# Optimization experiments

Measured on AMD Instinct MI355X. Metric: run time of the kernel, lower is better.

Reference implementation:

```python
import jax, jax.numpy as jnp
import numpy as np

N = 262144      # number of 3D points
D = 128         # in_channels
NCLS = 20       # classes
M = 10          # num_prototype
EPS = 0.05      # sinkhorn epsilon
ITERS = 3       # sinkhorn iterations
GAMMA = 0.99    # EMA momentum
LN_EPS = 1e-5

def layer_norm(x, g, b):
    mu = jnp.mean(x, axis=-1, keepdims=True)
    v = jnp.mean((x - mu) ** 2, axis=-1, keepdims=True)
    return (x - mu) / jnp.sqrt(v + LN_EPS) * g + b

def l2n(x):
    # F.normalize(p=2, dim=-1) with eps=1e-12
    return x / jnp.clip(jnp.linalg.norm(x, axis=-1, keepdims=True), 1e-12)

def setup_inputs() -> dict:
    key = jax.random.key(0)
    k1, k2, k3 = jax.random.split(key, 3)
    return {
        "feature3d": jax.random.normal(k1, (N, D), dtype=jnp.float32),
        "gt_seg": jax.random.randint(k2, (N,), 0, NCLS, dtype=jnp.int32),
        "prototypes": jax.random.normal(k3, (NCLS, M, D), dtype=jnp.float32),
        "feat_gamma": jnp.ones((D,), jnp.float32),
        "feat_beta": jnp.zeros((D,), jnp.float32),
        "mask_gamma": jnp.ones((NCLS,), jnp.float32),
        "mask_beta": jnp.zeros((NCLS,), jnp.float32),
    }

def reference(feature3d, gt_seg, prototypes, feat_gamma, feat_beta, mask_gamma, mask_beta):
    _c = l2n(layer_norm(feature3d, feat_gamma, feat_beta))            # [N,D]
    protos = l2n(prototypes)                                          # [K,M,D]
    masks = jnp.einsum('nd,kmd->nmk', _c, protos)                     # [N,M,K]
    out_seg = layer_norm(jnp.max(masks, axis=1), mask_gamma, mask_beta)  # [N,K]

    # ---- prototype_learning ----
    pred = jnp.argmax(out_seg, axis=-1)
    correct = (gt_seg == pred).astype(_c.dtype)                       # [N]
    proto_logits = _c @ protos.reshape(-1, D).T                       # [N,K*M]

    sel = jax.nn.one_hot(gt_seg, NCLS, dtype=_c.dtype)                # [N,K]
    # masked per-class sinkhorn, vectorized across all 20 classes
    L = jnp.exp(jnp.transpose(masks, (2, 1, 0)) / EPS) * sel.T[:, None, :]  # [K,M,N]
    B = jnp.sum(sel, axis=0)                                          # [K] points per class
    s = jnp.sum(L, axis=(1, 2), keepdims=True)
    L = L / jnp.where(s > 0, s, 1.0)
    Bsafe = jnp.where(B > 0, B, 1.0)[:, None, None]
    for _ in range(ITERS):
        rs = jnp.sum(L, axis=2, keepdims=True)                        # per-prototype row sum
        L = L / (jnp.where(rs > 0, rs, 1.0) * M)
        cs = jnp.sum(L, axis=1, keepdims=True)                        # per-point col sum
        L = L / jnp.where(cs > 0, cs, 1.0) / Bsafe
    L = L * B[:, None, None]

    idx = jnp.argmax(L, axis=1)                                       # [K,N] hard assignment
    q = jax.nn.one_hot(idx, M, dtype=_c.dtype)                        # [K,N,M] (one_hot(argmax))

    w = sel.T * correct[None, :]                                      # [K,N] class-k AND correct
    m_q = q * w[:, :, None]                                           # [K,N,M]
    f = jnp.einsum('knm,nd->kmd', m_q, _c * correct[:, None])         # [K,M,D]
    ncount = jnp.sum(m_q, axis=1)                                     # [K,M]
    fn = l2n(f)
    upd = GAMMA * protos + (1.0 - GAMMA) * fn                         # momentum_update
    new_protos = l2n(jnp.where(ncount[..., None] > 0, upd, protos))   # [K,M,D]

    idx_pp = idx[gt_seg, jnp.arange(N)]                               # per-point proto index
    proto_target = (idx_pp + M * gt_seg).astype(jnp.float32)          # [N]
    return out_seg, proto_logits, proto_target, new_protos
```

## Files before the change

kernel.cpp:

```cpp
#include <hip/hip_runtime.h>
#include <hip/hip_bf16.h>

#define NPTS 262144
#define DIM  128
#define KC   20
#define MP   10
#define LNEPS 1e-5f
#define EPSI  0.05f
#define CCAP  65536

typedef _Float16 half8 __attribute__((ext_vector_type(8)));
typedef float f32x4 __attribute__((ext_vector_type(4)));
typedef float fv4 __attribute__((ext_vector_type(4)));

union H8U4 { half8 h; uint4 u; };

#define WS_PN     0
#define WS_PHI    25600
#define WS_PLO    39936
#define WS_F      54272
#define WS_NCOUNT 79872
#define WS_CCNT   80072
#define WS_UH     80080
#define WS_CS     80680
#define WS_PCB    80904
#define WS_EXPV   998408
#define WS_CIDX   3619848

#define EPIT 212

#define MFMA_(b_, a_, c_) __builtin_amdgcn_mfma_f32_16x16x32_f16(b_, a_, c_, 0, 0, 0)

__device__ __forceinline__ half8 lds_h8(const uint4* p) {
    return *reinterpret_cast<const half8*>(p);
}

__device__ __forceinline__ void gload_lds16(const uint4* g, uint4* l) {
    __builtin_amdgcn_global_load_lds(
        (const __attribute__((address_space(1))) void*)(g),
        (__attribute__((address_space(3))) void*)(l), 16, 0, 0);
}

__device__ __forceinline__ void nt_store4(float* p, float x, float y, float z, float w) {
    fv4 v = {x, y, z, w};
    __builtin_nontemporal_store(v, (fv4*)p);
}

__device__ __forceinline__ float class_S(const float* cs, int k) {
    float S = 0.f;
    #pragma unroll
    for (int m = 0; m < 10; ++m) S += cs[k*10 + m];
    return S;
}
__device__ __forceinline__ float u1_of(const float* cs, int j) {
    int k = j / 10;
    float S = class_S(cs, k);
    float r1 = (S > 0.f) ? cs[j] / S : cs[j];
    return (r1 > 0.f) ? 1.f/(10.f*r1) : 0.1f;
}

__global__ __launch_bounds__(64) void k_norm_protos(
    const float* __restrict__ pr, float* __restrict__ pn,
    _Float16* __restrict__ phi, _Float16* __restrict__ plo,
    float* __restrict__ zbuf)
{
    int j = blockIdx.x, l = threadIdx.x;
    {
        int tid = j*64 + l;
        for (int i = tid; i < 25808; i += 14336) zbuf[i] = 0.f;
    }
    const int jm = j & 15;
    const int s1 = l >> 3,       swz1 = (((s1 ^ jm) << 3) | (l & 7));
    const int s2 = 8 + (l >> 3), swz2 = (((s2 ^ jm) << 3) | (l & 7));
    if (j < 200) {
        float x0 = pr[(size_t)j*128 + l], x1 = pr[(size_t)j*128 + 64 + l];
        float ss = x0*x0 + x1*x1;
        #pragma unroll
        for (int off = 32; off > 0; off >>= 1) ss += __shfl_xor(ss, off);
        float dn = fmaxf(sqrtf(ss), 1e-12f);
        float y0 = x0/dn, y1 = x1/dn;
        pn[(size_t)j*128 + l]      = y0;
        pn[(size_t)j*128 + 64 + l] = y1;
        _Float16 h0 = (_Float16)y0, h1 = (_Float16)y1;
        phi[(size_t)j*128 + swz1] = h0;
        phi[(size_t)j*128 + swz2] = h1;
        plo[(size_t)j*128 + swz1] = (_Float16)(y0 - (float)h0);
        plo[(size_t)j*128 + swz2] = (_Float16)(y1 - (float)h1);
    } else {
        phi[(size_t)j*128 + swz1] = (_Float16)0.f;  phi[(size_t)j*128 + swz2] = (_Float16)0.f;
        plo[(size_t)j*128 + swz1] = (_Float16)0.f;  plo[(size_t)j*128 + swz2] = (_Float16)0.f;
    }
}

__global__ __launch_bounds__(256, 4) void k_main(
    const float* __restrict__ feat, const int* __restrict__ gt,
    const _Float16* __restrict__ phi, const _Float16* __restrict__ plo,
    const float* __restrict__ fg, const float* __restrict__ fb,
    const float* __restrict__ mg, const float* __restrict__ mb,
    float* __restrict__ out_seg, float* __restrict__ plog,
    float* __restrict__ expv, float* __restrict__ pcb,
    int* __restrict__ cidx, int* __restrict__ ccnt)
{
    __shared__ __align__(16) char ldsb[32768];
    uint4* bbuf = (uint4*)ldsb;
    float* epi  = (float*)ldsb;
    float* osg  = (float*)(ldsb + 27136);
    float* exs  = (float*)(ldsb + 29696);
    int*   gtS  = (int*)  (ldsb + 30976);
    float* part = (float*)(ldsb + 31232);
    float* cntS = (float*)(ldsb + 31872);

    const int t = threadIdx.x, blk = blockIdx.x;
    const int w = t >> 6, lane = t & 63;
    const int l15 = lane & 15, l4 = lane >> 4;
    const int pbase = blk * 64;

    const uint4* phi4 = (const uint4*)phi;
    const uint4* plo4 = (const uint4*)plo;

#define STAGE_B(S, BI) do { \
        const uint4* gh = phi4 + (size_t)(S)*512 + t; \
        const uint4* gl = plo4 + (size_t)(S)*512 + t; \
        uint4* dh = bbuf + (BI)*1024 + w*64; \
        uint4* dl = bbuf + (BI)*1024 + 512 + w*64; \
        gload_lds16(gh,       dh); \
        gload_lds16(gh + 256, dh + 256); \
        gload_lds16(gl,       dl); \
        gload_lds16(gl + 256, dl + 256); \
    } while (0)

#define EPI_WRITE(P) do { \
        int row = (w & 1)*16 + l15; \
        _Pragma("unroll") \
        for (int nt = 0; nt < 13; ++nt) \
            if (nt < 12 || l4 < 2) { \
                float4 sv; \
                sv.x = acc[nt][0]; sv.y = acc[nt][1]; \
                sv.z = acc[nt][2]; sv.w = acc[nt][3]; \
                *reinterpret_cast<float4*>(&epi[row*EPIT + nt*16 + l4*4]) = sv; \
            } \
    } while (0)

#define PASS_COMPUTE(P) do { \
        { \
            float* pdst = plog + (size_t)(pbase + (P)*32)*200; \
            _Pragma("unroll") \
            for (int it = 0; it < 7; ++it) { \
                int f = it*256 + t; \
                if (f < 1600) { \
                    int row = f / 50, c4 = f - row*50; \
                    const float* sp = &epi[row*EPIT + c4*4]; \
                    nt_store4(&pdst[(size_t)f*4], sp[0], sp[1], sp[2], sp[3]); \
                } \
            } \
        } \
        if (t < 128) { \
            const int q = t >> 2, sub = t & 3; \
            const int n = pbase + (P)*32 + q; \
            float ml[5]; \
            _Pragma("unroll") \
            for (int kk = 0; kk < 5; ++kk) { \
                int k = sub*5 + kk; \
                float mx = epi[q*EPIT + k*10]; \
                _Pragma("unroll") \
                for (int m = 1; m < 10; ++m) mx = fmaxf(mx, epi[q*EPIT + k*10 + m]); \
                ml[kk] = mx; \
            } \
            float s0 = ml[0]+ml[1]+ml[2]+ml[3]+ml[4]; \
            s0 += __shfl_xor(s0,1); s0 += __shfl_xor(s0,2); \
            float mean = s0 / 20.f; \
            float s1 = 0.f; \
            _Pragma("unroll") \
            for (int kk = 0; kk < 5; ++kk) { float d = ml[kk]-mean; s1 += d*d; } \
            s1 += __shfl_xor(s1,1); s1 += __shfl_xor(s1,2); \
            float rstd = rsqrtf(s1 / 20.f + LNEPS); \
            float bv = -1e30f; int bk = 0; \
            _Pragma("unroll") \
            for (int kk = 0; kk < 5; ++kk) { \
                int k = sub*5 + kk; \
                float y = (ml[kk]-mean)*rstd*mg[k] + mb[k]; \
                osg[q*20 + k] = y; \
                if (y > bv) { bv = y; bk = k; } \
            } \
            _Pragma("unroll") \
            for (int off = 1; off <= 2; off <<= 1) { \
                float ov = __shfl_xor(bv, off); \
                int   ok = __shfl_xor(bk, off); \
                if (ov > bv || (ov == bv && ok < bk)) { bv = ov; bk = ok; } \
            } \
            int g = gt[n]; \
            if (sub == 0) { \
                if (bk == g) { \
                    int slot = atomicAdd(ccnt, 1); \
                    if (slot < CCAP) cidx[slot] = n; \
                } \
                _Pragma("unroll") \
                for (int m = 0; m < 10; ++m) \
                    exs[q*10 + m] = expf(epi[q*EPIT + g*10 + m] / EPSI); \
                gtS[(P)*32 + q] = g; \
            } \
        } \
    } while (0)

#define PASS_STORE(P) do { \
        if (t < 160) { \
            const float* sp = &osg[t*4]; \
            nt_store4(&out_seg[(size_t)(pbase + (P)*32)*20 + t*4], sp[0], sp[1], sp[2], sp[3]); \
        } else if (t < 240) { \
            int f = t - 160; \
            *reinterpret_cast<float4*>(&expv[(size_t)(pbase + (P)*32)*10 + f*4]) \
                = *reinterpret_cast<const float4*>(&exs[f*4]); \
        } \
        if (t < 200) { \
            int kk = t / 10, mm = t - kk*10; \
            _Pragma("unroll 4") \
            for (int i = 0; i < 32; ++i) \
                if (gtS[(P)*32 + i] == kk) eacc += exs[i*10 + mm]; \
        } \
    } while (0)

    STAGE_B(0, 0);

    const float4* gfeat = (const float4*)feat;
    float4 A[4][2];
    {
        size_t rb = (size_t)(pbase + w*16 + l15) * 32;
        #pragma unroll
        for (int kst = 0; kst < 4; ++kst)
            #pragma unroll
            for (int h = 0; h < 2; ++h)
                A[kst][h] = gfeat[rb + kst*8 + l4*2 + h];
    }
    float4 G[4][2], Bb[4][2];
    {
        const float4* fg4 = (const float4*)fg;
        const float4* fb4 = (const float4*)fb;
        #pragma unroll
        for (int kst = 0; kst < 4; ++kst)
            #pragma unroll
            for (int h = 0; h < 2; ++h) {
                G[kst][h]  = fg4[kst*8 + l4*2 + h];
                Bb[kst][h] = fb4[kst*8 + l4*2 + h];
            }
    }

    half8 fah[4], fal[4];
    {
        float s0 = 0.f;
        #pragma unroll
        for (int kst = 0; kst < 4; ++kst)
            #pragma unroll
            for (int h = 0; h < 2; ++h) {
                float4 v = A[kst][h];
                s0 += v.x + v.y + v.z + v.w;
            }
        s0 += __shfl_xor(s0, 16); s0 += __shfl_xor(s0, 32);
        float mean = s0 * (1.f/128.f);
        float s1 = 0.f;
        #pragma unroll
        for (int kst = 0; kst < 4; ++kst)
            #pragma unroll
            for (int h = 0; h < 2; ++h) {
                float4 v = A[kst][h];
                float a = v.x-mean, b = v.y-mean, c = v.z-mean, d = v.w-mean;
                s1 += a*a + b*b + c*c + d*d;
            }
        s1 += __shfl_xor(s1, 16); s1 += __shfl_xor(s1, 32);
        float rstd = rsqrtf(s1 * (1.f/128.f) + LNEPS);
        float s2 = 0.f;
        #pragma unroll
        for (int kst = 0; kst < 4; ++kst)
            #pragma unroll
            for (int h = 0; h < 2; ++h) {
                float4 v = A[kst][h];
                float4 g = G[kst][h], bb = Bb[kst][h];
                v.x = (v.x-mean)*rstd*g.x + bb.x;
                v.y = (v.y-mean)*rstd*g.y + bb.y;
                v.z = (v.z-mean)*rstd*g.z + bb.z;
                v.w = (v.w-mean)*rstd*g.w + bb.w;
                A[kst][h] = v;
                s2 += v.x*v.x + v.y*v.y + v.z*v.z + v.w*v.w;
            }
        s2 += __shfl_xor(s2, 16); s2 += __shfl_xor(s2, 32);
        float rl2 = 1.f / fmaxf(sqrtf(s2), 1e-12f);
        #pragma unroll
        for (int kst = 0; kst < 4; ++kst) {
            float4 va = A[kst][0], vb = A[kst][1];
            va.x*=rl2; va.y*=rl2; va.z*=rl2; va.w*=rl2;
            vb.x*=rl2; vb.y*=rl2; vb.z*=rl2; vb.w*=rl2;
            H8U4 h, lo;
            h.h[0]=(_Float16)va.x; h.h[1]=(_Float16)va.y; h.h[2]=(_Float16)va.z; h.h[3]=(_Float16)va.w;
            h.h[4]=(_Float16)vb.x; h.h[5]=(_Float16)vb.y; h.h[6]=(_Float16)vb.z; h.h[7]=(_Float16)vb.w;
            lo.h[0]=(_Float16)(va.x-(float)h.h[0]); lo.h[1]=(_Float16)(va.y-(float)h.h[1]);
            lo.h[2]=(_Float16)(va.z-(float)h.h[2]); lo.h[3]=(_Float16)(va.w-(float)h.h[3]);
            lo.h[4]=(_Float16)(vb.x-(float)h.h[4]); lo.h[5]=(_Float16)(vb.y-(float)h.h[5]);
            lo.h[6]=(_Float16)(vb.z-(float)h.h[6]); lo.h[7]=(_Float16)(vb.w-(float)h.h[7]);
            fah[kst] = h.h;
            fal[kst] = lo.h;
        }
    }

    f32x4 acc[13];
    #pragma unroll
    for (int nt = 0; nt < 13; ++nt)
        acc[nt] = (f32x4){0.f,0.f,0.f,0.f};

    __syncthreads();

    #pragma unroll
    for (int s = 0; s < 7; ++s) {
        if (s < 6) STAGE_B(s + 1, (s + 1) & 1);
        const uint4* bb = bbuf + (s & 1)*1024;
        if (s < 6) {
            #pragma unroll
            for (int kst = 0; kst < 4; ++kst) {
                const int slz = (kst*4 + l4) ^ l15;
                half8 b0h = lds_h8(bb + l15*16 + slz);
                half8 b0l = lds_h8(bb + 512 + l15*16 + slz);
                half8 b1h = lds_h8(bb + (16+l15)*16 + slz);
                half8 b1l = lds_h8(bb + 512 + (16+l15)*16 + slz);
                acc[2*s]   = MFMA_(b0h, fah[kst], acc[2*s]);
                acc[2*s+1] = MFMA_(b1h, fah[kst], acc[2*s+1]);
                acc[2*s]   = MFMA_(b0h, fal[kst], acc[2*s]);
                acc[2*s+1] = MFMA_(b1h, fal[kst], acc[2*s+1]);
                acc[2*s]   = MFMA_(b0l, fah[kst], acc[2*s]);
                acc[2*s+1] = MFMA_(b1l, fah[kst], acc[2*s+1]);
                acc[2*s]   = MFMA_(b0l, fal[kst], acc[2*s]);
                acc[2*s+1] = MFMA_(b1l, fal[kst], acc[2*s+1]);
            }
        } else {
            #pragma unroll
            for (int kst = 0; kst < 4; ++kst) {
                const int slz = (kst*4 + l4) ^ l15;
                half8 b0h = lds_h8(bb + l15*16 + slz);
                half8 b0l = lds_h8(bb + 512 + l15*16 + slz);
                acc[12] = MFMA_(b0h, fah[kst], acc[12]);
                acc[12] = MFMA_(b0h, fal[kst], acc[12]);
                acc[12] = MFMA_(b0l, fah[kst], acc[12]);
                acc[12] = MFMA_(b0l, fal[kst], acc[12]);
            }
        }
        __syncthreads();
    }

    float eacc = 0.f;
    if ((w >> 1) == 0) EPI_WRITE(0);
    __syncthreads();
    PASS_COMPUTE(0);
    __syncthreads();
    PASS_STORE(0);
    if ((w >> 1) == 1) EPI_WRITE(1);
    __syncthreads();
    PASS_COMPUTE(1);
    __syncthreads();
    PASS_STORE(1);
    if (t < 160) {
        int c = t >> 3, o = t & 7;
        float cnt = 0.f;
        for (int i = o*8; i < o*8 + 8; ++i)
            if (gtS[i] == c) cnt += 1.f;
        part[t] = cnt;
    }
    __syncthreads();
    if (t < 20) {
        float cnt = 0.f;
        #pragma unroll
        for (int o = 0; o < 8; ++o) cnt += part[t*8+o];
        cntS[t] = cnt;
    }
    __syncthreads();
    if (t < 224)
        pcb[(size_t)blk*224 + t] = (t < 200) ? eacc : ((t < 220) ? cntS[t-200] : 0.f);
#undef STAGE_B
#undef EPI_WRITE
#undef PASS_COMPUTE
#undef PASS_STORE
}

__global__ __launch_bounds__(256) void k_red1a(
    const float* __restrict__ pcb, float* __restrict__ colsum)
{
    __shared__ float red[256];
    int t = threadIdx.x, col = blockIdx.x;
    float s = 0.f;
    #pragma unroll
    for (int i = 0; i < 16; ++i) s += pcb[(size_t)(i*256 + t)*224 + col];
    red[t] = s; __syncthreads();
    for (int off = 128; off > 0; off >>= 1) { if (t < off) red[t] += red[t+off]; __syncthreads(); }
    if (t == 0) colsum[col] = red[0];
}

__global__ __launch_bounds__(256) void k_row(int iter,
    const int* __restrict__ gt, const float* __restrict__ expv,
    const float* __restrict__ uh, const float* __restrict__ cs,
    float* __restrict__ pr)
{
    __shared__ float prodS[2560];
    __shared__ int gtS[256];
    __shared__ float uS[200], skS[20], BcS[20];
    int t = threadIdx.x, b = blockIdx.x;
    if (t < 20) {
        skS[t] = class_S(cs, t);
        BcS[t] = cs[200 + t];
    }
    if (t < 200) uS[t] = u1_of(cs, t);
    int n = b*256 + t;
    int g = gt[n];
    float e[10];
    {
        const float2* e2 = (const float2*)(expv + (size_t)n*10);
        float2 a0=e2[0], a1=e2[1], a2=e2[2], a3=e2[3], a4=e2[4];
        e[0]=a0.x; e[1]=a0.y; e[2]=a1.x; e[3]=a1.y; e[4]=a2.x;
        e[5]=a2.y; e[6]=a3.x; e[7]=a3.y; e[8]=a4.x; e[9]=a4.y;
    }
    __syncthreads();
    float skg = skS[g];
    float v = (skg > 0.f) ? 1.f/skg : 1.f;
    float B = BcS[g];
    float Bs = (B > 0.f) ? B : 1.f;
    {
        const float* uc = &uS[g*10];
        float sc = 0.f;
        #pragma unroll
        for (int m = 0; m < 10; ++m) sc += e[m]*uc[m];
        v = (sc > 0.f) ? 1.f/(Bs*sc) : v/Bs;
    }
    if (iter == 3) {
        const float* uc = uh + 200 + g*10;
        float sc = 0.f;
        #pragma unroll
        for (int m = 0; m < 10; ++m) sc += e[m]*uc[m];
        v = (sc > 0.f) ? 1.f/(Bs*sc) : v/Bs;
    }
    #pragma unroll
    for (int m = 0; m < 10; ++m) prodS[t*10+m] = e[m]*v;
    gtS[t] = g;
    __syncthreads();
    if (t < 200) {
        int kk = t / 10, mm = t % 10;
        float acc = 0.f;
        for (int i = 0; i < 256; ++i)
            if (gtS[i] == kk) acc += prodS[i*10+mm];
        pr[(size_t)t*1024 + b] = acc;
    }
}

__global__ __launch_bounds__(256) void k_reduce_u(int iter,
    const float* __restrict__ pr, const float* __restrict__ cs,
    float* __restrict__ uh)
{
    __shared__ float red[256];
    int t = threadIdx.x, j = blockIdx.x;
    float s = 0.f;
    #pragma unroll
    for (int i = 0; i < 4; ++i) s += pr[(size_t)j*1024 + i*256 + t];
    red[t] = s; __syncthreads();
    for (int off = 128; off > 0; off >>= 1) { if (t < off) red[t] += red[t+off]; __syncthreads(); }
    if (t == 0) {
        float S = red[0];
        float uprev = (iter == 2) ? u1_of(cs, j) : uh[(iter-2)*200 + j];
        uh[(iter-1)*200 + j] = (S > 0.f) ? 1.f/(10.f*S) : uprev*0.1f;
    }
}

__global__ __launch_bounds__(256) void k_post(
    const int* __restrict__ gt, const float* __restrict__ expv,
    const float* __restrict__ u,
    const int* __restrict__ cidx, const int* __restrict__ ccnt,
    const float* __restrict__ feat, const float* __restrict__ fg,
    const float* __restrict__ fb,
    float* __restrict__ ptarget, float* __restrict__ facc,
    float* __restrict__ ncount)
{
    int t = threadIdx.x;
    {
        int n = blockIdx.x*256 + t;
        int g = gt[n];
        const float* uk = u + g*10;
        const float2* e2 = (const float2*)(expv + (size_t)n*10);
        float bv = -1e30f; int idx = 0;
        #pragma unroll
        for (int m2 = 0; m2 < 5; ++m2) {
            float2 ev = e2[m2];
            float p0 = ev.x * uk[m2*2], p1 = ev.y * uk[m2*2+1];
            if (p0 > bv) { bv = p0; idx = m2*2; }
            if (p1 > bv) { bv = p1; idx = m2*2+1; }
        }
        ptarget[n] = (float)(idx + 10*g);
    }
    int wid = blockIdx.x*4 + (t >> 6);
    int lane = t & 63;
    int cnt = *ccnt; if (cnt > CCAP) cnt = CCAP;
    for (int i = wid; i < cnt; i += 4096) {
        int n = cidx[i];
        float x0 = feat[(size_t)n*128 + lane], x1 = feat[(size_t)n*128 + 64 + lane];
        float s = x0 + x1;
        #pragma unroll
        for (int off = 32; off > 0; off >>= 1) s += __shfl_xor(s, off);
        float mean = s * (1.f/128.f);
        float d0 = x0 - mean, d1 = x1 - mean;
        float s2 = d0*d0 + d1*d1;
        #pragma unroll
        for (int off = 32; off > 0; off >>= 1) s2 += __shfl_xor(s2, off);
        float rstd = rsqrtf(s2 * (1.f/128.f) + LNEPS);
        float y0 = d0*rstd*fg[lane] + fb[lane];
        float y1 = d1*rstd*fg[64+lane] + fb[64+lane];
        float s3 = y0*y0 + y1*y1;
        #pragma unroll
        for (int off = 32; off > 0; off >>= 1) s3 += __shfl_xor(s3, off);
        float rl2 = 1.f / fmaxf(sqrtf(s3), 1e-12f);
        float c0 = y0*rl2, c1 = y1*rl2;
        int g = gt[n];
        const float* uk = u + g*10;
        const float2* e2 = (const float2*)(expv + (size_t)n*10);
        float bv = -1e30f; int idx = 0;
        #pragma unroll
        for (int m2 = 0; m2 < 5; ++m2) {
            float2 ev = e2[m2];
            float p0 = ev.x * uk[m2*2], p1 = ev.y * uk[m2*2+1];
            if (p0 > bv) { bv = p0; idx = m2*2; }
            if (p1 > bv) { bv = p1; idx = m2*2+1; }
        }
        float* frow = facc + (size_t)(g*10+idx)*128;
        atomicAdd(&frow[lane], c0);
        atomicAdd(&frow[64+lane], c1);
        if (lane == 0) atomicAdd(&ncount[g*10+idx], 1.f);
    }
}

__global__ __launch_bounds__(64) void k_proto_update(
    const float* __restrict__ facc, const float* __restrict__ ncount,
    const float* __restrict__ pn, float* __restrict__ outp)
{
    const float OMG = (float)(1.0 - 0.99);
    int j = blockIdx.x, l = threadIdx.x;
    float f0 = facc[(size_t)j*128+l], f1 = facc[(size_t)j*128+64+l];
    float ss = f0*f0 + f1*f1;
    #pragma unroll
    for (int off = 32; off > 0; off >>= 1) ss += __shfl_xor(ss, off);
    float fl2 = fmaxf(sqrtf(ss), 1e-12f);
    float fn0 = f0/fl2, fn1 = f1/fl2;
    float p0 = pn[(size_t)j*128+l], p1 = pn[(size_t)j*128+64+l];
    float u0 = 0.99f*p0 + OMG*fn0, u1 = 0.99f*p1 + OMG*fn1;
    bool ok = ncount[j] > 0.f;
    float s0 = ok ? u0 : p0, s1 = ok ? u1 : p1;
    float ss2 = s0*s0 + s1*s1;
    #pragma unroll
    for (int off = 32; off > 0; off >>= 1) ss2 += __shfl_xor(ss2, off);
    float l2 = fmaxf(sqrtf(ss2), 1e-12f);
    outp[(size_t)j*128+l]      = s0/l2;
    outp[(size_t)j*128+64+l]   = s1/l2;
}

extern "C" void kernel_launch(void* const* d_in, const int* in_sizes, int n_in,
                              void* d_out, int out_size, void* d_ws, size_t ws_size,
                              hipStream_t stream)
{
    const float* feat   = (const float*)d_in[0];
    const int*   gt     = (const int*)  d_in[1];
    const float* protos = (const float*)d_in[2];
    const float* fg     = (const float*)d_in[3];
    const float* fb     = (const float*)d_in[4];
    const float* mg     = (const float*)d_in[5];
    const float* mb     = (const float*)d_in[6];

    float* out      = (float*)d_out;
    float* out_seg  = out;
    float* plog     = out + (size_t)NPTS*20;
    float* ptarget  = out + (size_t)NPTS*220;
    float* newp     = out + (size_t)NPTS*221;

    float* ws   = (float*)d_ws;
    float* pn   = ws + WS_PN;
    _Float16* phi = (_Float16*)(ws + WS_PHI);
    _Float16* plo = (_Float16*)(ws + WS_PLO);
    float* facc = ws + WS_F;
    float* ncnt = ws + WS_NCOUNT;
    int*   ccnt = (int*)(ws + WS_CCNT);
    float* uh   = ws + WS_UH;
    float* cs   = ws + WS_CS;
    float* pcb  = ws + WS_PCB;
    float* pr   = ws + WS_PCB;
    float* expv = ws + WS_EXPV;
    int*   cidx = (int*)(ws + WS_CIDX);

    hipLaunchKernelGGL(k_norm_protos, dim3(224), dim3(64), 0, stream,
                       protos, pn, phi, plo, facc);
    hipLaunchKernelGGL(k_main, dim3(4096), dim3(256), 0, stream,
                       feat, gt, phi, plo, fg, fb, mg, mb, out_seg, plog, expv, pcb,
                       cidx, ccnt);
    hipLaunchKernelGGL(k_red1a, dim3(220), dim3(256), 0, stream, pcb, cs);
    for (int it = 2; it <= 3; ++it) {
        hipLaunchKernelGGL(k_row, dim3(1024), dim3(256), 0, stream, it, gt, expv, uh, cs, pr);
        hipLaunchKernelGGL(k_reduce_u, dim3(200), dim3(256), 0, stream, it, pr, cs, uh);
    }
    hipLaunchKernelGGL(k_post, dim3(1024), dim3(256), 0, stream,
                       gt, expv, uh + 400, cidx, ccnt, feat, fg, fb, ptarget, facc, ncnt);
    hipLaunchKernelGGL(k_proto_update, dim3(200), dim3(64), 0, stream, facc, ncnt, pn, newp);
}
```

Baseline: 231.1 us.

## Process two 64-point tiles per block in k_main and prefetch next tile

Each k_main block now handles 128 points in two sequential 64-point passes, halving the grid to 2048 blocks and the per-block partial rows that k_red1a must reduce. The feature load for the second tile and the first prototype stage are issued before the first tile's epilogue so global latency overlaps with epilogue work. Class counts are carried across the two passes. Launch bounds drop to 3 waves per SIMD to give room for the extra live registers, which may lower occupancy.

```diff
diff --git a/kernel.cpp b/kernel.cpp
--- a/kernel.cpp
+++ b/kernel.cpp
@@ -92,7 +92,7 @@
     }
 }
 
-__global__ __launch_bounds__(256, 4) void k_main(
+__global__ __launch_bounds__(256, 3) void k_main(
     const float* __restrict__ feat, const int* __restrict__ gt,
     const _Float16* __restrict__ phi, const _Float16* __restrict__ plo,
     const float* __restrict__ fg, const float* __restrict__ fb,
@@ -113,10 +113,10 @@
     const int t = threadIdx.x, blk = blockIdx.x;
     const int w = t >> 6, lane = t & 63;
     const int l15 = lane & 15, l4 = lane >> 4;
-    const int pbase = blk * 64;
 
     const uint4* phi4 = (const uint4*)phi;
     const uint4* plo4 = (const uint4*)plo;
+    const float4* gfeat = (const float4*)feat;
 
 #define STAGE_B(S, BI) do { \
         const uint4* gh = phi4 + (size_t)(S)*512 + t; \
@@ -129,7 +129,123 @@
         gload_lds16(gl + 256, dl + 256); \
     } while (0)
 
-#define EPI_WRITE(P) do { \
+#define ALOAD(PB) do { \
+        size_t rb = (size_t)((PB) + w*16 + l15) * 32; \
+        _Pragma("unroll") \
+        for (int kst = 0; kst < 4; ++kst) \
+            _Pragma("unroll") \
+            for (int h = 0; h < 2; ++h) \
+                A[kst][h] = gfeat[rb + kst*8 + l4*2 + h]; \
+    } while (0)
+
+#define LN_BODY do { \
+        const float4* fg4 = (const float4*)fg; \
+        const float4* fb4 = (const float4*)fb; \
+        float4 G[4][2], Bb[4][2]; \
+        _Pragma("unroll") \
+        for (int kst = 0; kst < 4; ++kst) \
+            _Pragma("unroll") \
+            for (int h = 0; h < 2; ++h) { \
+                G[kst][h]  = fg4[kst*8 + l4*2 + h]; \
+                Bb[kst][h] = fb4[kst*8 + l4*2 + h]; \
+            } \
+        float s0 = 0.f; \
+        _Pragma("unroll") \
+        for (int kst = 0; kst < 4; ++kst) \
+            _Pragma("unroll") \
+            for (int h = 0; h < 2; ++h) { \
+                float4 v = A[kst][h]; \
+                s0 += v.x + v.y + v.z + v.w; \
+            } \
+        s0 += __shfl_xor(s0, 16); s0 += __shfl_xor(s0, 32); \
+        float mean = s0 * (1.f/128.f); \
+        float s1 = 0.f; \
+        _Pragma("unroll") \
+        for (int kst = 0; kst < 4; ++kst) \
+            _Pragma("unroll") \
+            for (int h = 0; h < 2; ++h) { \
+                float4 v = A[kst][h]; \
+                float a = v.x-mean, b = v.y-mean, c = v.z-mean, d = v.w-mean; \
+                s1 += a*a + b*b + c*c + d*d; \
+            } \
+        s1 += __shfl_xor(s1, 16); s1 += __shfl_xor(s1, 32); \
+        float rstd = rsqrtf(s1 * (1.f/128.f) + LNEPS); \
+        float s2 = 0.f; \
+        _Pragma("unroll") \
+        for (int kst = 0; kst < 4; ++kst) \
+            _Pragma("unroll") \
+            for (int h = 0; h < 2; ++h) { \
+                float4 v = A[kst][h]; \
+                float4 g = G[kst][h], bb = Bb[kst][h]; \
+                v.x = (v.x-mean)*rstd*g.x + bb.x; \
+                v.y = (v.y-mean)*rstd*g.y + bb.y; \
+                v.z = (v.z-mean)*rstd*g.z + bb.z; \
+                v.w = (v.w-mean)*rstd*g.w + bb.w; \
+                A[kst][h] = v; \
+                s2 += v.x*v.x + v.y*v.y + v.z*v.z + v.w*v.w; \
+            } \
+        s2 += __shfl_xor(s2, 16); s2 += __shfl_xor(s2, 32); \
+        float rl2 = 1.f / fmaxf(sqrtf(s2), 1e-12f); \
+        _Pragma("unroll") \
+        for (int kst = 0; kst < 4; ++kst) { \
+            float4 va = A[kst][0], vb = A[kst][1]; \
+            va.x*=rl2; va.y*=rl2; va.z*=rl2; va.w*=rl2; \
+            vb.x*=rl2; vb.y*=rl2; vb.z*=rl2; vb.w*=rl2; \
+            H8U4 h, lo; \
+            h.h[0]=(_Float16)va.x; h.h[1]=(_Float16)va.y; h.h[2]=(_Float16)va.z; h.h[3]=(_Float16)va.w; \
+            h.h[4]=(_Float16)vb.x; h.h[5]=(_Float16)vb.y; h.h[6]=(_Float16)vb.z; h.h[7]=(_Float16)vb.w; \
+            lo.h[0]=(_Float16)(va.x-(float)h.h[0]); lo.h[1]=(_Float16)(va.y-(float)h.h[1]); \
+            lo.h[2]=(_Float16)(va.z-(float)h.h[2]); lo.h[3]=(_Float16)(va.w-(float)h.h[3]); \
+            lo.h[4]=(_Float16)(vb.x-(float)h.h[4]); lo.h[5]=(_Float16)(vb.y-(float)h.h[5]); \
+            lo.h[6]=(_Float16)(vb.z-(float)h.h[6]); lo.h[7]=(_Float16)(vb.w-(float)h.h[7]); \
+            fah[kst] = h.h; \
+            fal[kst] = lo.h; \
+        } \
+    } while (0)
+
+#define GEMM_LOOP do { \
+        _Pragma("unroll") \
+        for (int nt = 0; nt < 13; ++nt) \
+            acc[nt] = (f32x4){0.f,0.f,0.f,0.f}; \
+        __syncthreads(); \
+        _Pragma("unroll") \
+        for (int s = 0; s < 7; ++s) { \
+            if (s < 6) STAGE_B(s + 1, (s + 1) & 1); \
+            const uint4* bb = bbuf + (s & 1)*1024; \
+            if (s < 6) { \
+                _Pragma("unroll") \
+                for (int kst = 0; kst < 4; ++kst) { \
+                    const int slz = (kst*4 + l4) ^ l15; \
+                    half8 b0h = lds_h8(bb + l15*16 + slz); \
+                    half8 b0l = lds_h8(bb + 512 + l15*16 + slz); \
+                    half8 b1h = lds_h8(bb + (16+l15)*16 + slz); \
+                    half8 b1l = lds_h8(bb + 512 + (16+l15)*16 + slz); \
+                    acc[2*s]   = MFMA_(b0h, fah[kst], acc[2*s]); \
+                    acc[2*s+1] = MFMA_(b1h, fah[kst], acc[2*s+1]); \
+                    acc[2*s]   = MFMA_(b0h, fal[kst], acc[2*s]); \
+                    acc[2*s+1] = MFMA_(b1h, fal[kst], acc[2*s+1]); \
+                    acc[2*s]   = MFMA_(b0l, fah[kst], acc[2*s]); \
+                    acc[2*s+1] = MFMA_(b1l, fah[kst], acc[2*s+1]); \
+                    acc[2*s]   = MFMA_(b0l, fal[kst], acc[2*s]); \
+                    acc[2*s+1] = MFMA_(b1l, fal[kst], acc[2*s+1]); \
+                } \
+            } else { \
+                _Pragma("unroll") \
+                for (int kst = 0; kst < 4; ++kst) { \
+                    const int slz = (kst*4 + l4) ^ l15; \
+                    half8 b0h = lds_h8(bb + l15*16 + slz); \
+                    half8 b0l = lds_h8(bb + 512 + l15*16 + slz); \
+                    acc[12] = MFMA_(b0h, fah[kst], acc[12]); \
+                    acc[12] = MFMA_(b0h, fal[kst], acc[12]); \
+                    acc[12] = MFMA_(b0l, fah[kst], acc[12]); \
+                    acc[12] = MFMA_(b0l, fal[kst], acc[12]); \
+                } \
+            } \
+            __syncthreads(); \
+        } \
+    } while (0)
+
+#define EPI_WRITE do { \
         int row = (w & 1)*16 + l15; \
         _Pragma("unroll") \
         for (int nt = 0; nt < 13; ++nt) \
@@ -219,137 +335,58 @@
         } \
     } while (0)
 
+    float4 A[4][2];
+    half8 fah[4], fal[4];
+    f32x4 acc[13];
+    float eacc = 0.f, ccum = 0.f;
+    int pbase = blk * 128;
+
     STAGE_B(0, 0);
-
-    const float4* gfeat = (const float4*)feat;
-    float4 A[4][2];
-    {
-        size_t rb = (size_t)(pbase + w*16 + l15) * 32;
-        #pragma unroll
-        for (int kst = 0; kst < 4; ++kst)
-            #pragma unroll
-            for (int h = 0; h < 2; ++h)
-                A[kst][h] = gfeat[rb + kst*8 + l4*2 + h];
-    }
-    float4 G[4][2], Bb[4][2];
-    {
-        const float4* fg4 = (const float4*)fg;
-        const float4* fb4 = (const float4*)fb;
-        #pragma unroll
-        for (int kst = 0; kst < 4; ++kst)
-            #pragma unroll
-            for (int h = 0; h < 2; ++h) {
-                G[kst][h]  = fg4[kst*8 + l4*2 + h];
-                Bb[kst][h] = fb4[kst*8 + l4*2 + h];
-            }
-    }
-
-    half8 fah[4], fal[4];
-    {
-        float s0 = 0.f;
-        #pragma unroll
-        for (int kst = 0; kst < 4; ++kst)
-            #pragma unroll
-            for (int h = 0; h < 2; ++h) {
-                float4 v = A[kst][h];
-                s0 += v.x + v.y + v.z + v.w;
-            }
-        s0 += __shfl_xor(s0, 16); s0 += __shfl_xor(s0, 32);
-        float mean = s0 * (1.f/128.f);
-        float s1 = 0.f;
-        #pragma unroll
-        for (int kst = 0; kst < 4; ++kst)
-            #pragma unroll
-            for (int h = 0; h < 2; ++h) {
-                float4 v = A[kst][h];
-                float a = v.x-mean, b = v.y-mean, c = v.z-mean, d = v.w-mean;
-                s1 += a*a + b*b + c*c + d*d;
-            }
-        s1 += __shfl_xor(s1, 16); s1 += __shfl_xor(s1, 32);
-        float rstd = rsqrtf(s1 * (1.f/128.f) + LNEPS);
-        float s2 = 0.f;
-        #pragma unroll
-        for (int kst = 0; kst < 4; ++kst)
-            #pragma unroll
-            for (int h = 0; h < 2; ++h) {
-                float4 v = A[kst][h];
-                float4 g = G[kst][h], bb = Bb[kst][h];
-                v.x = (v.x-mean)*rstd*g.x + bb.x;
-                v.y = (v.y-mean)*rstd*g.y + bb.y;
-                v.z = (v.z-mean)*rstd*g.z + bb.z;
-                v.w = (v.w-mean)*rstd*g.w + bb.w;
-                A[kst][h] = v;
-                s2 += v.x*v.x + v.y*v.y + v.z*v.z + v.w*v.w;
-            }
-        s2 += __shfl_xor(s2, 16); s2 += __shfl_xor(s2, 32);
-        float rl2 = 1.f / fmaxf(sqrtf(s2), 1e-12f);
-        #pragma unroll
-        for (int kst = 0; kst < 4; ++kst) {
-            float4 va = A[kst][0], vb = A[kst][1];
-            va.x*=rl2; va.y*=rl2; va.z*=rl2; va.w*=rl2;
-            vb.x*=rl2; vb.y*=rl2; vb.z*=rl2; vb.w*=rl2;
-            H8U4 h, lo;
-            h.h[0]=(_Float16)va.x; h.h[1]=(_Float16)va.y; h.h[2]=(_Float16)va.z; h.h[3]=(_Float16)va.w;
-            h.h[4]=(_Float16)vb.x; h.h[5]=(_Float16)vb.y; h.h[6]=(_Float16)vb.z; h.h[7]=(_Float16)vb.w;
-            lo.h[0]=(_Float16)(va.x-(float)h.h[0]); lo.h[1]=(_Float16)(va.y-(float)h.h[1]);
-            lo.h[2]=(_Float16)(va.z-(float)h.h[2]); lo.h[3]=(_Float16)(va.w-(float)h.h[3]);
-            lo.h[4]=(_Float16)(vb.x-(float)h.h[4]); lo.h[5]=(_Float16)(vb.y-(float)h.h[5]);
-            lo.h[6]=(_Float16)(vb.z-(float)h.h[6]); lo.h[7]=(_Float16)(vb.w-(float)h.h[7]);
-            fah[kst] = h.h;
-            fal[kst] = lo.h;
-        }
-    }
-
-    f32x4 acc[13];
-    #pragma unroll
-    for (int nt = 0; nt < 13; ++nt)
-        acc[nt] = (f32x4){0.f,0.f,0.f,0.f};
-
-    __syncthreads();
-
-    #pragma unroll
-    for (int s = 0; s < 7; ++s) {
-        if (s < 6) STAGE_B(s + 1, (s + 1) & 1);
-        const uint4* bb = bbuf + (s & 1)*1024;
-        if (s < 6) {
-            #pragma unroll
-            for (int kst = 0; kst < 4; ++kst) {
-                const int slz = (kst*4 + l4) ^ l15;
-                half8 b0h = lds_h8(bb + l15*16 + slz);
-                half8 b0l = lds_h8(bb + 512 + l15*16 + slz);
-                half8 b1h = lds_h8(bb + (16+l15)*16 + slz);
-                half8 b1l = lds_h8(bb + 512 + (16+l15)*16 + slz);
-                acc[2*s]   = MFMA_(b0h, fah[kst], acc[2*s]);
-                acc[2*s+1] = MFMA_(b1h, fah[kst], acc[2*s+1]);
-                acc[2*s]   = MFMA_(b0h, fal[kst], acc[2*s]);
-                acc[2*s+1] = MFMA_(b1h, fal[kst], acc[2*s+1]);
-                acc[2*s]   = MFMA_(b0l, fah[kst], acc[2*s]);
-                acc[2*s+1] = MFMA_(b1l, fah[kst], acc[2*s+1]);
-                acc[2*s]   = MFMA_(b0l, fal[kst], acc[2*s]);
-                acc[2*s+1] = MFMA_(b1l, fal[kst], acc[2*s+1]);
-            }
-        } else {
-            #pragma unroll
-            for (int kst = 0; kst < 4; ++kst) {
-                const int slz = (kst*4 + l4) ^ l15;
-                half8 b0h = lds_h8(bb + l15*16 + slz);
-                half8 b0l = lds_h8(bb + 512 + l15*16 + slz);
-                acc[12] = MFMA_(b0h, fah[kst], acc[12]);
-                acc[12] = MFMA_(b0h, fal[kst], acc[12]);
-                acc[12] = MFMA_(b0l, fah[kst], acc[12]);
-                acc[12] = MFMA_(b0l, fal[kst], acc[12]);
-            }
-        }
-        __syncthreads();
-    }
-
-    float eacc = 0.f;
-    if ((w >> 1) == 0) EPI_WRITE(0);
+    STAGE_B(1, 1);
+    ALOAD(pbase);
+    LN_BODY;
+    GEMM_LOOP;
+
+    ALOAD(pbase + 64);
+
+    if ((w >> 1) == 0) EPI_WRITE;
     __syncthreads();
     PASS_COMPUTE(0);
     __syncthreads();
     PASS_STORE(0);
-    if ((w >> 1) == 1) EPI_WRITE(1);
+    if ((w >> 1) == 1) EPI_WRITE;
+    __syncthreads();
+    PASS_COMPUTE(1);
+    __syncthreads();
+    PASS_STORE(1);
+    STAGE_B(0, 0);
+    if (t < 160) {
+        int c = t >> 3, o = t & 7;
+        float cnt = 0.f;
+        for (int i = o*8; i < o*8 + 8; ++i)
+            if (gtS[i] == c) cnt += 1.f;
+        part[t] = cnt;
+    }
+    __syncthreads();
+    if (t < 20) {
+        float cnt = 0.f;
+        #pragma unroll
+        for (int o = 0; o < 8; ++o) cnt += part[t*8+o];
+        ccum += cnt;
+    }
+    __syncthreads();
+
+    pbase += 64;
+    STAGE_B(1, 1);
+    LN_BODY;
+    GEMM_LOOP;
+
+    if ((w >> 1) == 0) EPI_WRITE;
+    __syncthreads();
+    PASS_COMPUTE(0);
+    __syncthreads();
+    PASS_STORE(0);
+    if ((w >> 1) == 1) EPI_WRITE;
     __syncthreads();
     PASS_COMPUTE(1);
     __syncthreads();
@@ -366,12 +403,15 @@
         float cnt = 0.f;
         #pragma unroll
         for (int o = 0; o < 8; ++o) cnt += part[t*8+o];
-        cntS[t] = cnt;
+        cntS[t] = ccum + cnt;
     }
     __syncthreads();
     if (t < 224)
         pcb[(size_t)blk*224 + t] = (t < 200) ? eacc : ((t < 220) ? cntS[t-200] : 0.f);
 #undef STAGE_B
+#undef ALOAD
+#undef LN_BODY
+#undef GEMM_LOOP
 #undef EPI_WRITE
 #undef PASS_COMPUTE
 #undef PASS_STORE
@@ -384,7 +424,7 @@
     int t = threadIdx.x, col = blockIdx.x;
     float s = 0.f;
     #pragma unroll
-    for (int i = 0; i < 16; ++i) s += pcb[(size_t)(i*256 + t)*224 + col];
+    for (int i = 0; i < 8; ++i) s += pcb[(size_t)(i*256 + t)*224 + col];
     red[t] = s; __syncthreads();
     for (int off = 128; off > 0; off >>= 1) { if (t < off) red[t] += red[t+off]; __syncthreads(); }
     if (t == 0) colsum[col] = red[0];
@@ -586,7 +626,7 @@
 
     hipLaunchKernelGGL(k_norm_protos, dim3(224), dim3(64), 0, stream,
                        protos, pn, phi, plo, facc);
-    hipLaunchKernelGGL(k_main, dim3(4096), dim3(256), 0, stream,
+    hipLaunchKernelGGL(k_main, dim3(2048), dim3(256), 0, stream,
                        feat, gt, phi, plo, fg, fb, mg, mb, out_seg, plog, expv, pcb,
                        cidx, ccnt);
     hipLaunchKernelGGL(k_red1a, dim3(220), dim3(256), 0, stream, pcb, cs);
```

Result: slower. 250.6 us (+8.5%).
